# Performance work log

Measured on AMD Instinct MI355X. Metric: run time of the kernel, lower is better.

## Reference

```python
import jax, jax.numpy as jnp
import numpy as np

K = 3        # kernel size
PAD = 1      # padding
DG = 16      # deformable groups
MAXR = 10.0  # max_residue_magnitude


def _lrelu(x):
    return jnp.where(x >= 0, x, 0.1 * x)


def _conv3(x, w, b):
    y = jax.lax.conv_general_dilated(x, w, (1, 1), 'SAME',
                                     dimension_numbers=('NCHW', 'OIHW', 'NCHW'))
    return y + b[None, :, None, None]


def _deform_conv2d(x, offset, mask, weight, bias):
    # x: [B,Cin,H,W]; offset: [B,2*DG*K*K,H,W]; mask: [B,DG*K*K,H,W]
    B, Cin, H, W = x.shape
    Cout = weight.shape[0]
    G, Cg, K2 = DG, Cin // DG, K * K
    off = offset.reshape(B, G, K2, 2, H, W)
    dy, dx = off[:, :, :, 0], off[:, :, :, 1]
    ky = jnp.repeat(jnp.arange(K), K).astype(x.dtype)   # [K2]
    kx = jnp.tile(jnp.arange(K), K).astype(x.dtype)
    hh = jnp.arange(H, dtype=x.dtype)
    ww = jnp.arange(W, dtype=x.dtype)
    # sampling positions [B,G,K2,H,W]
    py = dy + ky[None, None, :, None, None] + hh[None, None, None, :, None] - PAD
    px = dx + kx[None, None, :, None, None] + ww[None, None, None, None, :] - PAD
    y0 = jnp.floor(py)
    x0 = jnp.floor(px)
    wy1 = py - y0
    wx1 = px - x0
    xf = x.reshape(B, G, Cg, H * W)

    def gather(yi, xi, wgt):
        valid = (yi >= 0) & (yi <= H - 1) & (xi >= 0) & (xi <= W - 1)
        idx = (jnp.clip(yi, 0, H - 1).astype(jnp.int32) * W
               + jnp.clip(xi, 0, W - 1).astype(jnp.int32)).reshape(B, G, -1)
        vals = jnp.take_along_axis(
            xf, jnp.broadcast_to(idx[:, :, None, :], (B, G, Cg, idx.shape[-1])), axis=3)
        vals = vals.reshape(B, G, Cg, K2, H, W)
        w = (wgt * valid.astype(x.dtype))[:, :, None]  # [B,G,1,K2,H,W]
        return vals * w

    s = (gather(y0, x0, (1 - wy1) * (1 - wx1))
         + gather(y0, x0 + 1, (1 - wy1) * wx1)
         + gather(y0 + 1, x0, wy1 * (1 - wx1))
         + gather(y0 + 1, x0 + 1, wy1 * wx1))
    s = s * mask.reshape(B, G, K2, H, W)[:, :, None]
    wr = weight.reshape(Cout, G, Cg, K2)
    out = jnp.einsum('ogck,bgckhw->bohw', wr, s)
    return out + bias[None, :, None, None]


def setup_inputs() -> dict:
    key = jax.random.key(0)
    ks = jax.random.split(key, 16)
    B, Cin, Cout, H, W = 4, 128, 64, 96, 96
    Coff = 3 * Cout + 4  # 196
    stdv = 1.0 / np.sqrt(Cin * K * K)
    inp = {
        'x': jax.random.normal(ks[0], (B, Cin, H, W), jnp.float32),
        'extra_feat': jax.random.normal(ks[1], (B, 3 * Cout, H, W), jnp.float32),
        'flow_1': jax.random.normal(ks[2], (B, 2, H, W), jnp.float32),
        'flow_2': jax.random.normal(ks[3], (B, 2, H, W), jnp.float32),
        'weight': jax.random.uniform(ks[4], (Cout, Cin, K, K), jnp.float32, -stdv, stdv),
        'bias': jax.random.normal(ks[5], (Cout,), jnp.float32) * 0.01,
        'ow0': jax.random.normal(ks[6], (Cout, Coff, K, K), jnp.float32) * 0.02,
        'ob0': jnp.zeros((Cout,), jnp.float32),
        'ow1': jax.random.normal(ks[7], (Cout, Cout, K, K), jnp.float32) * 0.02,
        'ob1': jnp.zeros((Cout,), jnp.float32),
        'ow2': jax.random.normal(ks[8], (Cout, Cout, K, K), jnp.float32) * 0.02,
        'ob2': jnp.zeros((Cout,), jnp.float32),
        'ow3': jax.random.normal(ks[9], (27 * DG, Cout, K, K), jnp.float32) * 0.01,
        'ob3': jnp.zeros((27 * DG,), jnp.float32),
    }
    return inp


def reference(x, extra_feat, flow_1, flow_2, weight, bias,
              ow0, ob0, ow1, ob1, ow2, ob2, ow3, ob3):
    feat = jnp.concatenate([extra_feat, flow_1, flow_2], axis=1)
    h = _lrelu(_conv3(feat, ow0, ob0))
    h = _lrelu(_conv3(h, ow1, ob1))
    h = _lrelu(_conv3(h, ow2, ob2))
    out = _conv3(h, ow3, ob3)
    o1, o2, m = jnp.split(out, 3, axis=1)
    offs = MAXR * jnp.tanh(jnp.concatenate([o1, o2], axis=1))
    off1, off2 = jnp.split(offs, 2, axis=1)
    off1 = off1 + jnp.tile(flow_1[:, ::-1], (1, off1.shape[1] // 2, 1, 1))
    off2 = off2 + jnp.tile(flow_2[:, ::-1], (1, off2.shape[1] // 2, 1, 1))
    offset = jnp.concatenate([off1, off2], axis=1)
    mask = jax.nn.sigmoid(m)
    return _deform_conv2d(x, offset, mask, weight, bias)
```

## Files before the change

### kernel.cpp

```cpp
#include <hip/hip_runtime.h>
#include <math.h>

#define HW 9216
#define Hh 96
#define Ww 96
#define PHW 9604

typedef __attribute__((ext_vector_type(8))) short bh8;
typedef __attribute__((ext_vector_type(4))) short bh4;
typedef __attribute__((ext_vector_type(4))) float f32x4;
typedef __attribute__((ext_vector_type(2))) float f32x2;

__device__ __forceinline__ short f2bf(float f) {
    union { float f; unsigned u; } v; v.f = f;
    unsigned r = v.u + 0x7FFFu + ((v.u >> 16) & 1u);
    return (short)(r >> 16);
}
__device__ __forceinline__ float bf2f(short s) {
    union { unsigned u; float f; } v; v.u = ((unsigned)(unsigned short)s) << 16;
    return v.f;
}

__global__ void zero_borders(short* __restrict__ xpad1,
                             short* __restrict__ hpa,
                             short* __restrict__ hpb) {
    int i = blockIdx.x * 256 + threadIdx.x;
    const int n1 = 4 * 388 * 224, n2 = 4 * 388 * 64;
    short* p; int C;
    if (i < n1) { p = xpad1; C = 224; }
    else if (i < n1 + n2) { p = hpa; C = 64; i -= n1; }
    else if (i < n1 + 2 * n2) { p = hpb; C = 64; i -= n1 + n2; }
    else return;
    int c = i % C;
    int r = i / C;
    int b = r / 388, pid = r - b * 388;
    int row, col;
    if (pid < 98)       { row = 0;  col = pid; }
    else if (pid < 196) { row = 97; col = pid - 98; }
    else if (pid < 292) { row = pid - 196 + 1; col = 0; }
    else                { row = pid - 292 + 1; col = 97; }
    p[((size_t)b * PHW + row * 98 + col) * C + c] = 0;
}

__global__ void pack_x1(const float* __restrict__ extra,
                        const float* __restrict__ f1,
                        const float* __restrict__ f2,
                        short* __restrict__ xp) {
    __shared__ float t[32][33];
    const int tid = threadIdx.x, tx = tid & 31, ty = tid >> 5;
    const int pt = blockIdx.x, ct = blockIdx.y, b = blockIdx.z;
#pragma unroll
    for (int j = 0; j < 4; ++j) {
        int ch = ct * 32 + ty + j * 8;
        int p = pt * 32 + tx;
        float v = 0.f;
        if (ch < 192)      v = extra[(b * 192 + ch) * HW + p];
        else if (ch < 194) v = f1[(b * 2 + ch - 192) * HW + p];
        else if (ch < 196) v = f2[(b * 2 + ch - 194) * HW + p];
        t[ty + j * 8][tx] = v;
    }
    __syncthreads();
#pragma unroll
    for (int j = 0; j < 4; ++j) {
        int pr = ty + j * 8;
        int p = pt * 32 + pr;
        int r = p / 96, c = p - r * 96;
        xp[((size_t)b * PHW + (r + 1) * 98 + (c + 1)) * 224 + ct * 32 + tx] =
            f2bf(t[tx][pr]);
    }
}

__global__ void pack_xd(const float* __restrict__ x, short* __restrict__ xd) {
    __shared__ float t[32][33];
    const int tid = threadIdx.x, tx = tid & 31, ty = tid >> 5;
    const int pt = blockIdx.x, ct = blockIdx.y, b = blockIdx.z;
#pragma unroll
    for (int j = 0; j < 4; ++j) {
        int ch = ct * 32 + ty + j * 8;
        t[ty + j * 8][tx] = x[((size_t)b * 128 + ch) * HW + pt * 32 + tx];
    }
    __syncthreads();
    if (tid < 128) {
        int oct = tid >> 5, p = tid & 31;
        int g = (ct * 32 + oct * 8) >> 3;
        bh8 v;
#pragma unroll
        for (int c = 0; c < 8; ++c) v[c] = f2bf(t[oct * 8 + c][p]);
        *(bh8*)&xd[(((size_t)b * 16 + g) * HW + pt * 32 + p) * 8] = v;
    }
}

__global__ void prep_weights(const float* __restrict__ ow0, const float* __restrict__ ow1,
                             const float* __restrict__ ow2, const float* __restrict__ ow3,
                             const float* __restrict__ wd,
                             short* __restrict__ wb0, short* __restrict__ wb1,
                             short* __restrict__ wb2, short* __restrict__ wb3,
                             short* __restrict__ wbd) {
    int i = blockIdx.x * 256 + threadIdx.x;
    const int n0 = 64 * 9 * 224, n1 = 64 * 9 * 64, n3 = 448 * 9 * 64, nd = 64 * 1152;
    if (i < n0) {
        int co = i / (9 * 224); int r = i - co * (9 * 224);
        int tap = r / 224, ci = r - tap * 224;
        wb0[i] = f2bf(ci < 196 ? ow0[(co * 196 + ci) * 9 + tap] : 0.f);
        return;
    }
    i -= n0;
    if (i < n1) {
        int co = i / (9 * 64); int r = i - co * (9 * 64);
        int tap = r / 64, ci = r - tap * 64;
        wb1[i] = f2bf(ow1[(co * 64 + ci) * 9 + tap]);
        return;
    }
    i -= n1;
    if (i < n1) {
        int co = i / (9 * 64); int r = i - co * (9 * 64);
        int tap = r / 64, ci = r - tap * 64;
        wb2[i] = f2bf(ow2[(co * 64 + ci) * 9 + tap]);
        return;
    }
    i -= n1;
    if (i < n3) {
        int co = i / (9 * 64); int r = i - co * (9 * 64);
        int tap = r / 64, ci = r - tap * 64;
        wb3[i] = f2bf(co < 432 ? ow3[(co * 64 + ci) * 9 + tap] : 0.f);
        return;
    }
    i -= n3;
    if (i < nd) {
        int co = i / 1152, kd = i - co * 1152;
        int gt = kd >> 3, c = kd & 7;
        int g = gt / 9, tap = gt - g * 9;
        wbd[i] = f2bf(wd[(co * 128 + g * 8 + c) * 9 + tap]);
    }
}

template<int CINP, int KCH>
__launch_bounds__(256)
__global__ void conv_mfma(const short* __restrict__ xp,
                          const short* __restrict__ wb,
                          const float* __restrict__ bias,
                          short* __restrict__ o1) {
    __shared__ __attribute__((aligned(16))) short smA[9 * 64 * 32];
    const int tid = threadIdx.x;
    const int lane = tid & 63, wv = tid >> 6;
    const int q = lane >> 4, l15 = lane & 15;
    const int b = blockIdx.y;
    const int strip = wv >> 1, coh = wv & 1;
    const int pix0 = blockIdx.x * 32 + strip * 16;
    const int soh = pix0 / 96, sow = pix0 - (pix0 / 96) * 96;

    const short* bp = xp + ((size_t)b * PHW + soh * 98 + sow + l15) * CINP + q * 8;

    const int sco = tid >> 2, sqq = tid & 3;
    const short* wsrc = wb + (size_t)sco * (9 * CINP) + sqq * 8;

    f32x4 acc[2];
#pragma unroll
    for (int t = 0; t < 2; ++t) acc[t] = (f32x4){0.f, 0.f, 0.f, 0.f};

    for (int p = 0; p < KCH; ++p) {
        __syncthreads();
        bh8 wtmp[9];
#pragma unroll
        for (int tap = 0; tap < 9; ++tap)
            wtmp[tap] = *(const bh8*)(wsrc + tap * CINP + p * 32);
#pragma unroll
        for (int tap = 0; tap < 9; ++tap)
            *(bh8*)&smA[tap * 2048 + sco * 32 + sqq * 8] = wtmp[tap];
        __syncthreads();
#pragma unroll
        for (int tap = 0; tap < 9; ++tap) {
            const int ky = tap / 3, kx = tap - (tap / 3) * 3;
            bh8 bf = *(const bh8*)(bp + (ky * 98 + kx) * CINP + p * 32);
#pragma unroll
            for (int t = 0; t < 2; ++t) {
                bh8 af = *(const bh8*)&smA[tap * 2048 + ((coh * 2 + t) * 16 + l15) * 32 + q * 8];
                acc[t] = __builtin_amdgcn_mfma_f32_16x16x32_bf16(af, bf, acc[t], 0, 0, 0);
            }
        }
    }

    size_t base = ((size_t)b * PHW + (soh + 1) * 98 + sow + l15 + 1) * 64;
#pragma unroll
    for (int t = 0; t < 2; ++t) {
        bh4 v4;
#pragma unroll
        for (int r = 0; r < 4; ++r) {
            int co = coh * 32 + t * 16 + q * 4 + r;
            float v = acc[t][r] + bias[co];
            v = (v >= 0.f) ? v : 0.1f * v;
            v4[r] = f2bf(v);
        }
        *(bh4*)(o1 + base + coh * 32 + t * 16 + q * 4) = v4;
    }
}

__launch_bounds__(256)
__global__ void conv4_gemm(const short* __restrict__ xp,
                           const short* __restrict__ wb,
                           const float* __restrict__ bias,
                           float* __restrict__ offp,
                           short* __restrict__ maskb,
                           const float* __restrict__ flow1,
                           const float* __restrict__ flow2) {
    __shared__ __attribute__((aligned(16))) short smA[64 * 64];
    __shared__ __attribute__((aligned(16))) short smB[192 * 64];
    const int tid = threadIdx.x;
    const int lane = tid & 63, wv = tid >> 6;
    const int q = lane >> 4, l15 = lane & 15;
    const int pg = blockIdx.x;
    const int b = blockIdx.y;
    const int cob = blockIdx.z * 64;
    const int r0 = pg * 2;

    f32x4 acc[3][4];
#pragma unroll
    for (int pf = 0; pf < 3; ++pf)
#pragma unroll
        for (int cf = 0; cf < 4; ++cf) acc[pf][cf] = (f32x4){0.f, 0.f, 0.f, 0.f};

    for (int tap = 0; tap < 9; ++tap) {
        const int ky = tap / 3, kx = tap - (tap / 3) * 3;
        __syncthreads();
#pragma unroll
        for (int it = 0; it < 2; ++it) {
            int id = it * 256 + tid;
            int row = id >> 3, s = id & 7;
            int sw = s ^ (row & 7);
            *(bh8*)&smA[row * 64 + sw * 8] =
                *(const bh8*)(wb + (size_t)(cob + row) * 576 + tap * 64 + s * 8);
        }
#pragma unroll
        for (int it = 0; it < 6; ++it) {
            int id = it * 256 + tid;
            int row = id >> 3, s = id & 7;
            int sw = s ^ (row & 7);
            int srow = (row >= 96) ? 1 : 0;
            int scol = row - srow * 96;
            *(bh8*)&smB[row * 64 + sw * 8] = *(const bh8*)&xp[
                ((size_t)b * PHW + (r0 + srow + ky) * 98 + scol + kx) * 64 + s * 8];
        }
        __syncthreads();
#pragma unroll
        for (int kc = 0; kc < 2; ++kc) {
            bh8 bf[3], af[4];
#pragma unroll
            for (int pf = 0; pf < 3; ++pf) {
                int row = wv * 48 + pf * 16 + l15;
                int sw = (kc * 4 + q) ^ (row & 7);
                bf[pf] = *(const bh8*)&smB[row * 64 + sw * 8];
            }
#pragma unroll
            for (int cf = 0; cf < 4; ++cf) {
                int row = cf * 16 + l15;
                int sw = (kc * 4 + q) ^ (row & 7);
                af[cf] = *(const bh8*)&smA[row * 64 + sw * 8];
            }
#pragma unroll
            for (int pf = 0; pf < 3; ++pf)
#pragma unroll
                for (int cf = 0; cf < 4; ++cf)
                    acc[pf][cf] = __builtin_amdgcn_mfma_f32_16x16x32_bf16(
                        af[cf], bf[pf], acc[pf][cf], 0, 0, 0);
        }
    }

#pragma unroll
    for (int pf = 0; pf < 3; ++pf) {
        int local = wv * 48 + pf * 16 + l15;
        int lrow = (local >= 96) ? 1 : 0;
        int pix = (r0 + lrow) * 96 + (local - lrow * 96);
#pragma unroll
        for (int cf = 0; cf < 4; ++cf) {
            int cb0 = cob + cf * 16 + q * 4;
            if (cb0 < 288) {
                const float* fl = (cb0 < 144) ? flow1 : flow2;
                float fe = fl[(b * 2 + 1) * HW + pix];
                float fo = fl[(b * 2) * HW + pix];
                float t0 = 10.f * tanhf(acc[pf][cf][0] + bias[cb0 + 0]) + fe;
                float t1 = 10.f * tanhf(acc[pf][cf][1] + bias[cb0 + 1]) + fo;
                float t2 = 10.f * tanhf(acc[pf][cf][2] + bias[cb0 + 2]) + fe;
                float t3 = 10.f * tanhf(acc[pf][cf][3] + bias[cb0 + 3]) + fo;
                size_t p0 = ((size_t)b * 144 + (cb0 >> 1)) * HW + pix;
                *(f32x2*)&offp[p0 * 2] = (f32x2){t0, t1};
                *(f32x2*)&offp[(p0 + HW) * 2] = (f32x2){t2, t3};
            } else {
#pragma unroll
                for (int r = 0; r < 4; ++r) {
                    int chn = cb0 + r;
                    if (chn < 432) {
                        float v = acc[pf][cf][r] + bias[chn];
                        maskb[((size_t)b * 144 + (chn - 288)) * HW + pix] =
                            f2bf(1.f / (1.f + expf(-v)));
                    }
                }
            }
        }
    }
}

__global__ void deform_mfma(const short* __restrict__ xd,
                            const float* __restrict__ offp,
                            const short* __restrict__ maskb,
                            const short* __restrict__ wbd,
                            const float* __restrict__ bias,
                            float* __restrict__ out) {
    __shared__ float red[4][1024];
    const int tid = threadIdx.x;
    const int lane = tid & 63, wv = tid >> 6;
    const int q = lane >> 4, l15 = lane & 15;
    const int blk = blockIdx.x;
    const int xs = blk & 7, idx = blk >> 3;
    const int b = xs >> 1;
    const int pix0 = ((xs & 1) * 288 + idx) * 16;
    const int pix = pix0 + l15;
    const int h = pix / 96, w = pix - (pix / 96) * 96;

    const float* opp = offp + ((size_t)b * 144 * HW + pix) * 2;
    const short* mp = maskb + (size_t)b * 144 * HW + pix;
    const short* xb = xd + (size_t)b * 16 * HW * 8;
    const short* ap = wbd + (size_t)l15 * 1152 + wv * 288 + q * 8;

    f32x2 dxy[9];
    float mk[9];
#pragma unroll
    for (int i = 0; i < 9; ++i) {
        const int gt = wv * 36 + i * 4 + q;
        dxy[i] = *(const f32x2*)(opp + (size_t)gt * HW * 2);
        mk[i] = bf2f(mp[(size_t)gt * HW]);
    }

    f32x4 acc[4];
#pragma unroll
    for (int t = 0; t < 4; ++t) acc[t] = (f32x4){0.f, 0.f, 0.f, 0.f};

#pragma unroll
    for (int i = 0; i < 9; ++i) {
        const int gt = wv * 36 + i * 4 + q;
        const int g = gt / 9, tap = gt - (gt / 9) * 9;
        float py = dxy[i][0] + (float)(tap / 3) + (float)h - 1.f;
        float px = dxy[i][1] + (float)(tap - (tap / 3) * 3) + (float)w - 1.f;
        float y0f = floorf(py), x0f = floorf(px);
        float wy1 = py - y0f, wx1 = px - x0f;
        float wy0 = 1.f - wy1, wx0 = 1.f - wx1;
        int y0 = (int)y0f, x0 = (int)x0f;
        int y1 = y0 + 1, x1 = x0 + 1;
        bool vy0 = (y0 >= 0) && (y0 < Hh), vy1 = (y1 >= 0) && (y1 < Hh);
        bool vx0 = (x0 >= 0) && (x0 < Ww), vx1 = (x1 >= 0) && (x1 < Ww);
        int cy0 = min(max(y0, 0), Hh - 1), cy1 = min(max(y1, 0), Hh - 1);
        int cx0 = min(max(x0, 0), Ww - 1), cx1 = min(max(x1, 0), Ww - 1);
        float m = mk[i];
        float w00 = wy0 * wx0 * ((vy0 && vx0) ? m : 0.f);
        float w01 = wy0 * wx1 * ((vy0 && vx1) ? m : 0.f);
        float w10 = wy1 * wx0 * ((vy1 && vx0) ? m : 0.f);
        float w11 = wy1 * wx1 * ((vy1 && vx1) ? m : 0.f);
        const short* cb = xb + (size_t)g * HW * 8;
        bh8 a00 = *(const bh8*)(cb + (size_t)(cy0 * 96 + cx0) * 8);
        bh8 a01 = *(const bh8*)(cb + (size_t)(cy0 * 96 + cx1) * 8);
        bh8 a10 = *(const bh8*)(cb + (size_t)(cy1 * 96 + cx0) * 8);
        bh8 a11 = *(const bh8*)(cb + (size_t)(cy1 * 96 + cx1) * 8);
        bh8 bf;
#pragma unroll
        for (int c = 0; c < 8; ++c) {
            float s = w00 * bf2f(a00[c]) + w01 * bf2f(a01[c])
                    + w10 * bf2f(a10[c]) + w11 * bf2f(a11[c]);
            bf[c] = f2bf(s);
        }
#pragma unroll
        for (int t = 0; t < 4; ++t) {
            bh8 af = *(const bh8*)(ap + (size_t)t * 16 * 1152 + i * 32);
            acc[t] = __builtin_amdgcn_mfma_f32_16x16x32_bf16(af, bf, acc[t], 0, 0, 0);
        }
    }

#pragma unroll
    for (int t = 0; t < 4; ++t)
#pragma unroll
        for (int r = 0; r < 4; ++r)
            red[wv][(t * 16 + q * 4 + r) * 16 + l15] = acc[t][r];
    __syncthreads();
    for (int e = tid; e < 1024; e += 256) {
        int co = e >> 4, pl = e & 15;
        float v = red[0][e] + red[1][e] + red[2][e] + red[3][e] + bias[co];
        out[((size_t)b * 64 + co) * HW + pix0 + pl] = v;
    }
}

extern "C" void kernel_launch(void* const* d_in, const int* in_sizes, int n_in,
                              void* d_out, int out_size, void* d_ws, size_t ws_size,
                              hipStream_t stream) {
    const float* x      = (const float*)d_in[0];
    const float* extra  = (const float*)d_in[1];
    const float* flow1  = (const float*)d_in[2];
    const float* flow2  = (const float*)d_in[3];
    const float* weight = (const float*)d_in[4];
    const float* bias   = (const float*)d_in[5];
    const float* ow0    = (const float*)d_in[6];
    const float* ob0    = (const float*)d_in[7];
    const float* ow1    = (const float*)d_in[8];
    const float* ob1    = (const float*)d_in[9];
    const float* ow2    = (const float*)d_in[10];
    const float* ob2    = (const float*)d_in[11];
    const float* ow3    = (const float*)d_in[12];
    const float* ob3    = (const float*)d_in[13];
    float* out = (float*)d_out;

    char* wsb = (char*)d_ws;
    short* xpad1 = (short*)wsb;   wsb += (size_t)4 * PHW * 224 * 2;
    short* hpa   = (short*)wsb;   wsb += (size_t)4 * PHW * 64 * 2;
    short* hpb   = (short*)wsb;   wsb += (size_t)4 * PHW * 64 * 2;
    float* offpair = (float*)wsb; wsb += (size_t)4 * 144 * HW * 2 * 4;
    short* maskbuf = (short*)wsb; wsb += (size_t)4 * 144 * HW * 2;
    short* xd      = (short*)wsb; wsb += (size_t)4 * 16 * HW * 8 * 2 + 32;
    short* wb0     = (short*)wsb; wsb += 64 * 9 * 224 * 2;
    short* wb1     = (short*)wsb; wsb += 64 * 9 * 64 * 2;
    short* wb2     = (short*)wsb; wsb += 64 * 9 * 64 * 2;
    short* wb3     = (short*)wsb; wsb += 448 * 9 * 64 * 2;
    short* wbd     = (short*)wsb;

    auto g1 = [](int n) { return dim3((n + 255) / 256); };
    zero_borders<<<g1(4 * 388 * 352), 256, 0, stream>>>(xpad1, hpa, hpb);
    pack_x1<<<dim3(288, 7, 4), 256, 0, stream>>>(extra, flow1, flow2, xpad1);
    pack_xd<<<dim3(288, 4, 4), 256, 0, stream>>>(x, xd);
    prep_weights<<<g1(534528), 256, 0, stream>>>(ow0, ow1, ow2, ow3, weight,
                                                 wb0, wb1, wb2, wb3, wbd);

    conv_mfma<224, 7><<<dim3(288, 4), 256, 0, stream>>>(xpad1, wb0, ob0, hpa);
    conv_mfma<64, 2><<<dim3(288, 4), 256, 0, stream>>>(hpa, wb1, ob1, hpb);
    conv_mfma<64, 2><<<dim3(288, 4), 256, 0, stream>>>(hpb, wb2, ob2, hpa);
    conv4_gemm<<<dim3(48, 4, 7), 256, 0, stream>>>(hpa, wb3, ob3, offpair,
                                                   maskbuf, flow1, flow2);
    deform_mfma<<<dim3(2304), 256, 0, stream>>>(xd, offpair, maskbuf, wbd, bias, out);
}
```

Baseline: 333.5 us.

## Pad deform input, merge prep kernels, widen conv tiles per wave

The deformable input is stored with a zero one-pixel border. Sampling positions are clamped to [-1,96], so the bilinear gather no longer needs per-corner validity checks or index clamping, and the four corners sit at fixed strides from one base pointer. The bf16 interpolation now works on packed 32-bit pairs. The border-zeroing and weight-prep kernels are merged into one launch, as are the two input-pack kernels, to cut launch count. Each conv wave now computes all 64 output channels for 16 pixels, which halves the grid and doubles the accumulators, trading occupancy and parallelism for reuse of the B fragment.

```diff
diff --git a/kernel.cpp b/kernel.cpp
--- a/kernel.cpp
+++ b/kernel.cpp
@@ -10,6 +10,8 @@
 typedef __attribute__((ext_vector_type(4))) short bh4;
 typedef __attribute__((ext_vector_type(4))) float f32x4;
 typedef __attribute__((ext_vector_type(2))) float f32x2;
+typedef __attribute__((ext_vector_type(4))) int i32x4;
+union bh8i { bh8 v; i32x4 i; };
 
 __device__ __forceinline__ short f2bf(float f) {
     union { float f; unsigned u; } v; v.f = f;
@@ -20,83 +22,61 @@
     union { unsigned u; float f; } v; v.u = ((unsigned)(unsigned short)s) << 16;
     return v.f;
 }
-
-__global__ void zero_borders(short* __restrict__ xpad1,
-                             short* __restrict__ hpa,
-                             short* __restrict__ hpb) {
+__device__ __forceinline__ float lo_bf(unsigned u) {
+    union { unsigned u; float f; } v; v.u = u << 16; return v.f;
+}
+__device__ __forceinline__ float hi_bf(unsigned u) {
+    union { unsigned u; float f; } v; v.u = u & 0xFFFF0000u; return v.f;
+}
+__device__ __forceinline__ unsigned pack_bf2(float lo, float hi) {
+    union { float f; unsigned u; } a, b; a.f = lo; b.f = hi;
+    unsigned ul = a.u + 0x7FFFu + ((a.u >> 16) & 1u);
+    unsigned uh = b.u + 0x7FFFu + ((b.u >> 16) & 1u);
+    return (ul >> 16) | (uh & 0xFFFF0000u);
+}
+
+__global__ void prep_misc(short* __restrict__ xpad1, short* __restrict__ hpa,
+                          short* __restrict__ hpb, short* __restrict__ xdp,
+                          const float* __restrict__ ow0, const float* __restrict__ ow1,
+                          const float* __restrict__ ow2, const float* __restrict__ ow3,
+                          const float* __restrict__ wd,
+                          short* __restrict__ wb0, short* __restrict__ wb1,
+                          short* __restrict__ wb2, short* __restrict__ wb3,
+                          short* __restrict__ wbd) {
     int i = blockIdx.x * 256 + threadIdx.x;
-    const int n1 = 4 * 388 * 224, n2 = 4 * 388 * 64;
-    short* p; int C;
-    if (i < n1) { p = xpad1; C = 224; }
-    else if (i < n1 + n2) { p = hpa; C = 64; i -= n1; }
-    else if (i < n1 + 2 * n2) { p = hpb; C = 64; i -= n1 + n2; }
-    else return;
-    int c = i % C;
-    int r = i / C;
-    int b = r / 388, pid = r - b * 388;
-    int row, col;
-    if (pid < 98)       { row = 0;  col = pid; }
-    else if (pid < 196) { row = 97; col = pid - 98; }
-    else if (pid < 292) { row = pid - 196 + 1; col = 0; }
-    else                { row = pid - 292 + 1; col = 97; }
-    p[((size_t)b * PHW + row * 98 + col) * C + c] = 0;
-}
-
-__global__ void pack_x1(const float* __restrict__ extra,
-                        const float* __restrict__ f1,
-                        const float* __restrict__ f2,
-                        short* __restrict__ xp) {
-    __shared__ float t[32][33];
-    const int tid = threadIdx.x, tx = tid & 31, ty = tid >> 5;
-    const int pt = blockIdx.x, ct = blockIdx.y, b = blockIdx.z;
-#pragma unroll
-    for (int j = 0; j < 4; ++j) {
-        int ch = ct * 32 + ty + j * 8;
-        int p = pt * 32 + tx;
-        float v = 0.f;
-        if (ch < 192)      v = extra[(b * 192 + ch) * HW + p];
-        else if (ch < 194) v = f1[(b * 2 + ch - 192) * HW + p];
-        else if (ch < 196) v = f2[(b * 2 + ch - 194) * HW + p];
-        t[ty + j * 8][tx] = v;
-    }
-    __syncthreads();
-#pragma unroll
-    for (int j = 0; j < 4; ++j) {
-        int pr = ty + j * 8;
-        int p = pt * 32 + pr;
-        int r = p / 96, c = p - r * 96;
-        xp[((size_t)b * PHW + (r + 1) * 98 + (c + 1)) * 224 + ct * 32 + tx] =
-            f2bf(t[tx][pr]);
-    }
-}
-
-__global__ void pack_xd(const float* __restrict__ x, short* __restrict__ xd) {
-    __shared__ float t[32][33];
-    const int tid = threadIdx.x, tx = tid & 31, ty = tid >> 5;
-    const int pt = blockIdx.x, ct = blockIdx.y, b = blockIdx.z;
-#pragma unroll
-    for (int j = 0; j < 4; ++j) {
-        int ch = ct * 32 + ty + j * 8;
-        t[ty + j * 8][tx] = x[((size_t)b * 128 + ch) * HW + pt * 32 + tx];
-    }
-    __syncthreads();
-    if (tid < 128) {
-        int oct = tid >> 5, p = tid & 31;
-        int g = (ct * 32 + oct * 8) >> 3;
-        bh8 v;
-#pragma unroll
-        for (int c = 0; c < 8; ++c) v[c] = f2bf(t[oct * 8 + c][p]);
-        *(bh8*)&xd[(((size_t)b * 16 + g) * HW + pt * 32 + p) * 8] = v;
-    }
-}
-
-__global__ void prep_weights(const float* __restrict__ ow0, const float* __restrict__ ow1,
-                             const float* __restrict__ ow2, const float* __restrict__ ow3,
-                             const float* __restrict__ wd,
-                             short* __restrict__ wb0, short* __restrict__ wb1,
-                             short* __restrict__ wb2, short* __restrict__ wb3,
-                             short* __restrict__ wbd) {
-    int i = blockIdx.x * 256 + threadIdx.x;
+    const int z1 = 4 * 388 * 224, z2 = 4 * 388 * 64;
+    if (i < z1 + 2 * z2) {
+        short* p; int C;
+        if (i < z1) { p = xpad1; C = 224; }
+        else if (i < z1 + z2) { p = hpa; C = 64; i -= z1; }
+        else { p = hpb; C = 64; i -= z1 + z2; }
+        int c = i % C;
+        int r = i / C;
+        int b = r / 388, pid = r - b * 388;
+        int row, col;
+        if (pid < 98)       { row = 0;  col = pid; }
+        else if (pid < 196) { row = 97; col = pid - 98; }
+        else if (pid < 292) { row = pid - 196 + 1; col = 0; }
+        else                { row = pid - 292 + 1; col = 97; }
+        p[((size_t)b * PHW + row * 98 + col) * C + c] = 0;
+        return;
+    }
+    i -= z1 + 2 * z2;
+    const int zr = 4 * 16 * 388 * 8;
+    if (i < zr) {
+        int c8 = i & 7;
+        int r = i >> 3;
+        int pid = r % 388;
+        int bg = r / 388;
+        int row, col;
+        if (pid < 98)       { row = 0;  col = pid; }
+        else if (pid < 196) { row = 97; col = pid - 98; }
+        else if (pid < 292) { row = pid - 196 + 1; col = 0; }
+        else                { row = pid - 292 + 1; col = 97; }
+        xdp[((size_t)bg * PHW + row * 98 + col) * 8 + c8] = 0;
+        return;
+    }
+    i -= zr;
     const int n0 = 64 * 9 * 224, n1 = 64 * 9 * 64, n3 = 448 * 9 * 64, nd = 64 * 1152;
     if (i < n0) {
         int co = i / (9 * 224); int r = i - co * (9 * 224);
@@ -131,6 +111,57 @@
         int gt = kd >> 3, c = kd & 7;
         int g = gt / 9, tap = gt - g * 9;
         wbd[i] = f2bf(wd[(co * 128 + g * 8 + c) * 9 + tap]);
+    }
+}
+
+__global__ void pack_all(const float* __restrict__ extra,
+                         const float* __restrict__ f1,
+                         const float* __restrict__ f2,
+                         const float* __restrict__ x,
+                         short* __restrict__ xp,
+                         short* __restrict__ xdp) {
+    __shared__ float t[32][33];
+    const int tid = threadIdx.x, tx = tid & 31, ty = tid >> 5;
+    const int pt = blockIdx.x, b = blockIdx.z;
+    if (blockIdx.y < 7) {
+        const int ct = blockIdx.y;
+#pragma unroll
+        for (int j = 0; j < 4; ++j) {
+            int ch = ct * 32 + ty + j * 8;
+            int p = pt * 32 + tx;
+            float v = 0.f;
+            if (ch < 192)      v = extra[(b * 192 + ch) * HW + p];
+            else if (ch < 194) v = f1[(b * 2 + ch - 192) * HW + p];
+            else if (ch < 196) v = f2[(b * 2 + ch - 194) * HW + p];
+            t[ty + j * 8][tx] = v;
+        }
+        __syncthreads();
+#pragma unroll
+        for (int j = 0; j < 4; ++j) {
+            int pr = ty + j * 8;
+            int p = pt * 32 + pr;
+            int r = p / 96, c = p - r * 96;
+            xp[((size_t)b * PHW + (r + 1) * 98 + (c + 1)) * 224 + ct * 32 + tx] =
+                f2bf(t[tx][pr]);
+        }
+    } else {
+        const int ct = blockIdx.y - 7;
+#pragma unroll
+        for (int j = 0; j < 4; ++j) {
+            int ch = ct * 32 + ty + j * 8;
+            t[ty + j * 8][tx] = x[((size_t)b * 128 + ch) * HW + pt * 32 + tx];
+        }
+        __syncthreads();
+        if (tid < 128) {
+            int oct = tid >> 5, p = tid & 31;
+            int g = ct * 4 + oct;
+            int pix = pt * 32 + p;
+            int r = pix / 96, c = pix - r * 96;
+            bh8 v;
+#pragma unroll
+            for (int cc = 0; cc < 8; ++cc) v[cc] = f2bf(t[oct * 8 + cc][p]);
+            *(bh8*)&xdp[(((size_t)b * 16 + g) * PHW + (r + 1) * 98 + (c + 1)) * 8] = v;
+        }
     }
 }
 
@@ -145,8 +176,7 @@
     const int lane = tid & 63, wv = tid >> 6;
     const int q = lane >> 4, l15 = lane & 15;
     const int b = blockIdx.y;
-    const int strip = wv >> 1, coh = wv & 1;
-    const int pix0 = blockIdx.x * 32 + strip * 16;
+    const int pix0 = blockIdx.x * 64 + wv * 16;
     const int soh = pix0 / 96, sow = pix0 - (pix0 / 96) * 96;
 
     const short* bp = xp + ((size_t)b * PHW + soh * 98 + sow + l15) * CINP + q * 8;
@@ -154,9 +184,9 @@
     const int sco = tid >> 2, sqq = tid & 3;
     const short* wsrc = wb + (size_t)sco * (9 * CINP) + sqq * 8;
 
-    f32x4 acc[2];
-#pragma unroll
-    for (int t = 0; t < 2; ++t) acc[t] = (f32x4){0.f, 0.f, 0.f, 0.f};
+    f32x4 acc[4];
+#pragma unroll
+    for (int t = 0; t < 4; ++t) acc[t] = (f32x4){0.f, 0.f, 0.f, 0.f};
 
     for (int p = 0; p < KCH; ++p) {
         __syncthreads();
@@ -173,8 +203,8 @@
             const int ky = tap / 3, kx = tap - (tap / 3) * 3;
             bh8 bf = *(const bh8*)(bp + (ky * 98 + kx) * CINP + p * 32);
 #pragma unroll
-            for (int t = 0; t < 2; ++t) {
-                bh8 af = *(const bh8*)&smA[tap * 2048 + ((coh * 2 + t) * 16 + l15) * 32 + q * 8];
+            for (int t = 0; t < 4; ++t) {
+                bh8 af = *(const bh8*)&smA[tap * 2048 + (t * 16 + l15) * 32 + q * 8];
                 acc[t] = __builtin_amdgcn_mfma_f32_16x16x32_bf16(af, bf, acc[t], 0, 0, 0);
             }
         }
@@ -182,16 +212,16 @@
 
     size_t base = ((size_t)b * PHW + (soh + 1) * 98 + sow + l15 + 1) * 64;
 #pragma unroll
-    for (int t = 0; t < 2; ++t) {
+    for (int t = 0; t < 4; ++t) {
         bh4 v4;
 #pragma unroll
         for (int r = 0; r < 4; ++r) {
-            int co = coh * 32 + t * 16 + q * 4 + r;
+            int co = t * 16 + q * 4 + r;
             float v = acc[t][r] + bias[co];
             v = (v >= 0.f) ? v : 0.1f * v;
             v4[r] = f2bf(v);
         }
-        *(bh4*)(o1 + base + coh * 32 + t * 16 + q * 4) = v4;
+        *(bh4*)(o1 + base + t * 16 + q * 4) = v4;
     }
 }
 
@@ -299,7 +329,8 @@
     }
 }
 
-__global__ void deform_mfma(const short* __restrict__ xd,
+__launch_bounds__(256)
+__global__ void deform_mfma(const short* __restrict__ xdp,
                             const float* __restrict__ offp,
                             const short* __restrict__ maskb,
                             const short* __restrict__ wbd,
@@ -318,7 +349,7 @@
 
     const float* opp = offp + ((size_t)b * 144 * HW + pix) * 2;
     const short* mp = maskb + (size_t)b * 144 * HW + pix;
-    const short* xb = xd + (size_t)b * 16 * HW * 8;
+    const short* xb = xdp + (size_t)b * 16 * PHW * 8;
     const short* ap = wbd + (size_t)l15 * 1152 + wv * 288 + q * 8;
 
     f32x2 dxy[9];
@@ -330,46 +361,52 @@
         mk[i] = bf2f(mp[(size_t)gt * HW]);
     }
 
-    f32x4 acc[4];
-#pragma unroll
-    for (int t = 0; t < 4; ++t) acc[t] = (f32x4){0.f, 0.f, 0.f, 0.f};
-
+    const short* cp[9];
+    f32x4 ww[9];
 #pragma unroll
     for (int i = 0; i < 9; ++i) {
         const int gt = wv * 36 + i * 4 + q;
         const int g = gt / 9, tap = gt - (gt / 9) * 9;
         float py = dxy[i][0] + (float)(tap / 3) + (float)h - 1.f;
         float px = dxy[i][1] + (float)(tap - (tap / 3) * 3) + (float)w - 1.f;
+        py = fminf(fmaxf(py, -1.f), 96.f);
+        px = fminf(fmaxf(px, -1.f), 96.f);
         float y0f = floorf(py), x0f = floorf(px);
         float wy1 = py - y0f, wx1 = px - x0f;
         float wy0 = 1.f - wy1, wx0 = 1.f - wx1;
-        int y0 = (int)y0f, x0 = (int)x0f;
-        int y1 = y0 + 1, x1 = x0 + 1;
-        bool vy0 = (y0 >= 0) && (y0 < Hh), vy1 = (y1 >= 0) && (y1 < Hh);
-        bool vx0 = (x0 >= 0) && (x0 < Ww), vx1 = (x1 >= 0) && (x1 < Ww);
-        int cy0 = min(max(y0, 0), Hh - 1), cy1 = min(max(y1, 0), Hh - 1);
-        int cx0 = min(max(x0, 0), Ww - 1), cx1 = min(max(x1, 0), Ww - 1);
+        int yp = (int)y0f + 1, xp = (int)x0f + 1;
+        cp[i] = xb + ((size_t)g * PHW + yp * 98 + xp) * 8;
         float m = mk[i];
-        float w00 = wy0 * wx0 * ((vy0 && vx0) ? m : 0.f);
-        float w01 = wy0 * wx1 * ((vy0 && vx1) ? m : 0.f);
-        float w10 = wy1 * wx0 * ((vy1 && vx0) ? m : 0.f);
-        float w11 = wy1 * wx1 * ((vy1 && vx1) ? m : 0.f);
-        const short* cb = xb + (size_t)g * HW * 8;
-        bh8 a00 = *(const bh8*)(cb + (size_t)(cy0 * 96 + cx0) * 8);
-        bh8 a01 = *(const bh8*)(cb + (size_t)(cy0 * 96 + cx1) * 8);
-        bh8 a10 = *(const bh8*)(cb + (size_t)(cy1 * 96 + cx0) * 8);
-        bh8 a11 = *(const bh8*)(cb + (size_t)(cy1 * 96 + cx1) * 8);
-        bh8 bf;
-#pragma unroll
-        for (int c = 0; c < 8; ++c) {
-            float s = w00 * bf2f(a00[c]) + w01 * bf2f(a01[c])
-                    + w10 * bf2f(a10[c]) + w11 * bf2f(a11[c]);
-            bf[c] = f2bf(s);
+        ww[i] = (f32x4){wy0 * wx0 * m, wy0 * wx1 * m, wy1 * wx0 * m, wy1 * wx1 * m};
+    }
+
+    f32x4 acc[4];
+#pragma unroll
+    for (int t = 0; t < 4; ++t) acc[t] = (f32x4){0.f, 0.f, 0.f, 0.f};
+
+#pragma unroll
+    for (int i = 0; i < 9; ++i) {
+        bh8i c00, c01, c10, c11;
+        c00.v = *(const bh8*)(cp[i]);
+        c01.v = *(const bh8*)(cp[i] + 8);
+        c10.v = *(const bh8*)(cp[i] + 98 * 8);
+        c11.v = *(const bh8*)(cp[i] + 99 * 8);
+        const float w00 = ww[i][0], w01 = ww[i][1], w10 = ww[i][2], w11 = ww[i][3];
+        bh8i bf;
+#pragma unroll
+        for (int k = 0; k < 4; ++k) {
+            unsigned u00 = (unsigned)c00.i[k], u01 = (unsigned)c01.i[k];
+            unsigned u10 = (unsigned)c10.i[k], u11 = (unsigned)c11.i[k];
+            float lo = w00 * lo_bf(u00) + w01 * lo_bf(u01)
+                     + w10 * lo_bf(u10) + w11 * lo_bf(u11);
+            float hi = w00 * hi_bf(u00) + w01 * hi_bf(u01)
+                     + w10 * hi_bf(u10) + w11 * hi_bf(u11);
+            bf.i[k] = (int)pack_bf2(lo, hi);
         }
 #pragma unroll
         for (int t = 0; t < 4; ++t) {
             bh8 af = *(const bh8*)(ap + (size_t)t * 16 * 1152 + i * 32);
-            acc[t] = __builtin_amdgcn_mfma_f32_16x16x32_bf16(af, bf, acc[t], 0, 0, 0);
+            acc[t] = __builtin_amdgcn_mfma_f32_16x16x32_bf16(af, bf.v, acc[t], 0, 0, 0);
         }
     }
 
@@ -411,24 +448,23 @@
     short* hpb   = (short*)wsb;   wsb += (size_t)4 * PHW * 64 * 2;
     float* offpair = (float*)wsb; wsb += (size_t)4 * 144 * HW * 2 * 4;
     short* maskbuf = (short*)wsb; wsb += (size_t)4 * 144 * HW * 2;
-    short* xd      = (short*)wsb; wsb += (size_t)4 * 16 * HW * 8 * 2 + 32;
+    short* xdp     = (short*)wsb; wsb += (size_t)4 * 16 * PHW * 8 * 2 + 32;
     short* wb0     = (short*)wsb; wsb += 64 * 9 * 224 * 2;
     short* wb1     = (short*)wsb; wsb += 64 * 9 * 64 * 2;
     short* wb2     = (short*)wsb; wsb += 64 * 9 * 64 * 2;
     short* wb3     = (short*)wsb; wsb += 448 * 9 * 64 * 2;
     short* wbd     = (short*)wsb;
 
-    auto g1 = [](int n) { return dim3((n + 255) / 256); };
-    zero_borders<<<g1(4 * 388 * 352), 256, 0, stream>>>(xpad1, hpa, hpb);
-    pack_x1<<<dim3(288, 7, 4), 256, 0, stream>>>(extra, flow1, flow2, xpad1);
-    pack_xd<<<dim3(288, 4, 4), 256, 0, stream>>>(x, xd);
-    prep_weights<<<g1(534528), 256, 0, stream>>>(ow0, ow1, ow2, ow3, weight,
-                                                 wb0, wb1, wb2, wb3, wbd);
-
-    conv_mfma<224, 7><<<dim3(288, 4), 256, 0, stream>>>(xpad1, wb0, ob0, hpa);
-    conv_mfma<64, 2><<<dim3(288, 4), 256, 0, stream>>>(hpa, wb1, ob1, hpb);
-    conv_mfma<64, 2><<<dim3(288, 4), 256, 0, stream>>>(hpb, wb2, ob2, hpa);
+    const int prep_total = 546304 + 198656 + 534528;
+    prep_misc<<<dim3((prep_total + 255) / 256), 256, 0, stream>>>(
+        xpad1, hpa, hpb, xdp, ow0, ow1, ow2, ow3, weight,
+        wb0, wb1, wb2, wb3, wbd);
+    pack_all<<<dim3(288, 11, 4), 256, 0, stream>>>(extra, flow1, flow2, x, xpad1, xdp);
+
+    conv_mfma<224, 7><<<dim3(144, 4), 256, 0, stream>>>(xpad1, wb0, ob0, hpa);
+    conv_mfma<64, 2><<<dim3(144, 4), 256, 0, stream>>>(hpa, wb1, ob1, hpb);
+    conv_mfma<64, 2><<<dim3(144, 4), 256, 0, stream>>>(hpb, wb2, ob2, hpa);
     conv4_gemm<<<dim3(48, 4, 7), 256, 0, stream>>>(hpa, wb3, ob3, offpair,
                                                    maskbuf, flow1, flow2);
-    deform_mfma<<<dim3(2304), 256, 0, stream>>>(xd, offpair, maskbuf, wbd, bias, out);
-}
+    deform_mfma<<<dim3(2304), 256, 0, stream>>>(xdp, offpair, maskbuf, wbd, bias, out);
+}
```

After: 291.4 us. -12.6%, faster.
